# Kernel optimization log

Measured on AMD Instinct MI355X. Metric: run time of the kernel, lower is better.

The kernel has to match this reference:

```python
import jax, jax.numpy as jnp
import numpy as np
from jax import lax

ALPHA = 0.85
C1 = 0.01 ** 2
C2 = 0.03 ** 2


def _avg_pool3(x):
    # F.avg_pool2d(x, 3, 1, 1) with count_include_pad=True: zero-pad, divide by 9.
    s = lax.reduce_window(x, jnp.array(0.0, x.dtype), lax.add,
                          (1, 1, 3, 3), (1, 1, 1, 1),
                          [(0, 0), (0, 0), (1, 1), (1, 1)])
    return s / jnp.array(9.0, x.dtype)


def _ssim(x, y):
    mu_x = _avg_pool3(x)
    mu_y = _avg_pool3(y)
    sigma_x = jnp.clip(_avg_pool3(x * x) - mu_x * mu_x, 0.0, None)
    sigma_y = jnp.clip(_avg_pool3(y * y) - mu_y * mu_y, 0.0, None)
    sigma_xy = _avg_pool3(x * y) - mu_x * mu_y
    ssim_n = (2.0 * mu_x * mu_y + C1) * (2.0 * sigma_xy + C2)
    ssim_d = (mu_x * mu_x + mu_y * mu_y + C1) * (sigma_x + sigma_y + C2)
    return jnp.clip((1.0 - ssim_n / ssim_d) / 2.0, 0.0, 1.0)


def _warp_right(right_img, disp):
    # grid_sample(bilinear, border, align_corners=True) where y maps identically
    # to its own row -> a 1D horizontal bilinear gather at x_sample = x - disp.
    B, C, H, W = right_img.shape
    x_base = jnp.arange(W, dtype=disp.dtype).reshape(1, 1, 1, W)
    x_sample = x_base - disp                      # [B,1,H,W]
    xs = jnp.clip(x_sample, 0.0, W - 1.0)         # border padding
    x0 = jnp.floor(xs)
    w = xs - x0                                   # frac weight
    i0 = x0.astype(jnp.int32)
    i1 = jnp.minimum(i0 + 1, W - 1)
    i0b = jnp.broadcast_to(i0, (B, C, H, W))
    i1b = jnp.broadcast_to(i1, (B, C, H, W))
    g0 = jnp.take_along_axis(right_img, i0b, axis=3)
    g1 = jnp.take_along_axis(right_img, i1b, axis=3)
    warped = (1.0 - w) * g0 + w * g1              # w broadcasts over C
    valid = ((x_sample > 0) & (x_sample < W - 1)).astype(disp.dtype)
    return warped, valid


def setup_inputs() -> dict:
    key = jax.random.key(0)
    k1, k2, k3 = jax.random.split(key, 3)
    B, H, W = 8, 720, 1280
    disp = jax.random.normal(k1, (B, 1, H, W), dtype=jnp.float32)
    left_img = jax.random.uniform(k2, (B, 3, H, W), dtype=jnp.float32)
    right_img = jax.random.uniform(k3, (B, 3, H, W), dtype=jnp.float32)
    return {"disp": disp, "left_img": left_img, "right_img": right_img}


def reference(disp, left_img, right_img):
    right_warped, valid = _warp_right(right_img, disp)
    l1_err = jnp.mean(jnp.abs(left_img - right_warped), axis=1, keepdims=True)
    ssim_err = jnp.mean(_ssim(left_img, right_warped), axis=1, keepdims=True)
    photo_err = ALPHA * ssim_err + (1.0 - ALPHA) * l1_err
    n_valid = jnp.maximum(jnp.sum(valid), 1.0)
    return jnp.sum(photo_err * valid) / n_valid
```

## Files before the change

### kernel.cpp

```cpp
#include <hip/hip_runtime.h>


#define P_ALPHA 0.85f
#define P_C1 1e-4f
#define P_C2 9e-4f

constexpr int COLS  = 62;
constexpr int RPW   = 12;
constexpr int WAVES = 4;

__global__ __launch_bounds__(256)
void photo_loss_kernel(const float* __restrict__ disp,
                       const float* __restrict__ left,
                       const float* __restrict__ right,
                       float* __restrict__ acc,
                       int H, int W)
{
    __shared__ float redpv[WAVES];
    __shared__ float redv[WAVES];

    const int tid  = threadIdx.x;
    const int lane = tid & 63;
    const int w    = tid >> 6;
    const int b    = blockIdx.z;
    const int col  = blockIdx.x * COLS + lane - 1;
    const int rowStart = (blockIdx.y * WAVES + w) * RPW;

    const int planeHW = H * W;
    const float* __restrict__ dispb = disp  + b * planeHW;
    const float* __restrict__ L0 = left  + (b * 3 + 0) * planeHW;
    const float* __restrict__ L1 = left  + (b * 3 + 1) * planeHW;
    const float* __restrict__ L2 = left  + (b * 3 + 2) * planeHW;
    const float* __restrict__ R0 = right + (b * 3 + 0) * planeHW;
    const float* __restrict__ R1 = right + (b * 3 + 1) * planeHW;
    const float* __restrict__ R2 = right + (b * 3 + 2) * planeHW;

    const float wm1f = (float)(W - 1);
    const int   colC = min(max(col, 0), W - 1);
    const float colv = (col >= 0 && col < W) ? 1.f : 0.f;
    const float ocm  = (lane >= 1 && lane <= COLS && col < W) ? 1.f : 0.f;

    float rsx[3][3], rsy[3][3], rsxx[3][3], rsyy[3][3], rsxy[3][3];
    float l1r[3], vr[3];

    float sum_pv = 0.f, sum_v = 0.f;

    auto emit = [&](int cs) {
        const float inv9 = 1.f / 9.f;
        float ssim_sum = 0.f;
        #pragma unroll
        for (int c = 0; c < 3; ++c) {
            float mu_x = (rsx[c][0]  + rsx[c][1]  + rsx[c][2])  * inv9;
            float mu_y = (rsy[c][0]  + rsy[c][1]  + rsy[c][2])  * inv9;
            float exx  = (rsxx[c][0] + rsxx[c][1] + rsxx[c][2]) * inv9;
            float eyy  = (rsyy[c][0] + rsyy[c][1] + rsyy[c][2]) * inv9;
            float exy  = (rsxy[c][0] + rsxy[c][1] + rsxy[c][2]) * inv9;
            float sig_x  = fmaxf(exx - mu_x * mu_x, 0.f);
            float sig_y  = fmaxf(eyy - mu_y * mu_y, 0.f);
            float sig_xy = exy - mu_x * mu_y;
            float n  = (2.f * mu_x * mu_y + P_C1) * (2.f * sig_xy + P_C2);
            float dd = (mu_x * mu_x + mu_y * mu_y + P_C1) * (sig_x + sig_y + P_C2);
            float s  = (1.f - n * __builtin_amdgcn_rcpf(dd)) * 0.5f;
            s = fminf(fmaxf(s, 0.f), 1.f);
            ssim_sum += s;
        }
        float photo = P_ALPHA * (ssim_sum * (1.f / 3.f))
                    + (1.f - P_ALPHA) * (l1r[cs] * (1.f / 3.f));
        sum_pv += photo * vr[cs] * ocm;
        sum_v  += vr[cs] * ocm;
    };

    float dC, xC0, xC1, xC2;
    {
        const int r  = rowStart - 1;
        const int rc = min(max(r, 0), H - 1);
        const int off = rc * W + colC;
        dC = dispb[off]; xC0 = L0[off]; xC1 = L1[off]; xC2 = L2[off];
    }

    #pragma unroll
    for (int j = 0; j <= RPW + 2; ++j) {
        const int s = j % 3;
        const int r = rowStart - 1 + j;
        if (j <= RPW + 1) {
            const int   rc = min(max(r, 0), H - 1);
            const float rv = (r >= 0 && r < H) ? 1.f : 0.f;
            const float m  = rv * colv;

            const float xs  = (float)col - dC;
            const float xcl = fminf(fmaxf(xs, 0.f), wm1f);
            const float xf  = floorf(xcl);
            const float fr  = xcl - xf;
            const int   i0  = (int)xf;
            const int   i1  = min(i0 + 1, W - 1);
            const int   ro  = rc * W;
            const float g00 = R0[ro + i0], g01 = R0[ro + i1];
            const float g10 = R1[ro + i0], g11 = R1[ro + i1];
            const float g20 = R2[ro + i0], g21 = R2[ro + i1];

            float dN = 0.f, xN0 = 0.f, xN1 = 0.f, xN2 = 0.f;
            if (j <= RPW) {
                const int rn   = min(max(r + 1, 0), H - 1);
                const int offn = rn * W + colC;
                dN = dispb[offn]; xN0 = L0[offn]; xN1 = L1[offn]; xN2 = L2[offn];
            }

            if (j >= 3) emit((s + 1) % 3);

            const float omf = 1.f - fr;
            const float y0 = (omf * g00 + fr * g01) * m;
            const float y1 = (omf * g10 + fr * g11) * m;
            const float y2 = (omf * g20 + fr * g21) * m;
            const float x0 = xC0 * m;
            const float x1 = xC1 * m;
            const float x2 = xC2 * m;

            float xl, xr, yl, yr;
            xl = __shfl_up(x0, 1, 64); xr = __shfl_down(x0, 1, 64);
            yl = __shfl_up(y0, 1, 64); yr = __shfl_down(y0, 1, 64);
            rsx[0][s]  = xl + x0 + xr;
            rsy[0][s]  = yl + y0 + yr;
            rsxx[0][s] = xl * xl + x0 * x0 + xr * xr;
            rsyy[0][s] = yl * yl + y0 * y0 + yr * yr;
            rsxy[0][s] = xl * yl + x0 * y0 + xr * yr;

            xl = __shfl_up(x1, 1, 64); xr = __shfl_down(x1, 1, 64);
            yl = __shfl_up(y1, 1, 64); yr = __shfl_down(y1, 1, 64);
            rsx[1][s]  = xl + x1 + xr;
            rsy[1][s]  = yl + y1 + yr;
            rsxx[1][s] = xl * xl + x1 * x1 + xr * xr;
            rsyy[1][s] = yl * yl + y1 * y1 + yr * yr;
            rsxy[1][s] = xl * yl + x1 * y1 + xr * yr;

            xl = __shfl_up(x2, 1, 64); xr = __shfl_down(x2, 1, 64);
            yl = __shfl_up(y2, 1, 64); yr = __shfl_down(y2, 1, 64);
            rsx[2][s]  = xl + x2 + xr;
            rsy[2][s]  = yl + y2 + yr;
            rsxx[2][s] = xl * xl + x2 * x2 + xr * xr;
            rsyy[2][s] = yl * yl + y2 * y2 + yr * yr;
            rsxy[2][s] = xl * yl + x2 * y2 + xr * yr;

            l1r[s] = fabsf(x0 - y0) + fabsf(x1 - y1) + fabsf(x2 - y2);
            vr[s]  = (xs > 0.f && xs < wm1f) ? 1.f : 0.f;

            dC = dN; xC0 = xN0; xC1 = xN1; xC2 = xN2;
        } else {
            emit((s + 1) % 3);
        }
    }

    #pragma unroll
    for (int off = 32; off > 0; off >>= 1) {
        sum_pv += __shfl_down(sum_pv, off, 64);
        sum_v  += __shfl_down(sum_v,  off, 64);
    }
    if (lane == 0) { redpv[w] = sum_pv; redv[w] = sum_v; }
    __syncthreads();
    if (tid == 0) {
        atomicAdd(&acc[0], redpv[0] + redpv[1] + redpv[2] + redpv[3]);
        atomicAdd(&acc[1], redv[0]  + redv[1]  + redv[2]  + redv[3]);
    }
}

__global__ void photo_loss_finalize(const float* __restrict__ acc,
                                    float* __restrict__ out)
{
    out[0] = acc[0] / fmaxf(acc[1], 1.f);
}

extern "C" void kernel_launch(void* const* d_in, const int* in_sizes, int n_in,
                              void* d_out, int out_size, void* d_ws, size_t ws_size,
                              hipStream_t stream)
{
    const float* disp  = (const float*)d_in[0];
    const float* left  = (const float*)d_in[1];
    const float* right = (const float*)d_in[2];
    float* out = (float*)d_out;
    float* acc = (float*)d_ws;

    const int B = 8, H = 720, W = 1280;

    hipMemsetAsync(acc, 0, 2 * sizeof(float), stream);

    dim3 grid((W + COLS - 1) / COLS, H / (WAVES * RPW), B);
    dim3 block(256);
    photo_loss_kernel<<<grid, block, 0, stream>>>(disp, left, right, acc, H, W);
    photo_loss_finalize<<<1, 1, 0, stream>>>(acc, out);
}
```

Before: 242.2 us.

## Flatten grid to per-wave tasks, process two tasks per wave, constant-fold sizes

Replaces the 3D grid with a 1D grid in which each wave independently takes two strip tasks (column strip × 12-row band × batch), so the number of blocks and atomics is halved. Image dimensions become compile-time constants, and the kernel asks for 5 blocks per SM through launch bounds. The goal is lower per-block launch and reduction overhead plus cheaper address arithmetic. In exchange, the larger register pressure limit may cause spills, and the decomposition of waves into tasks changes locality between neighbouring strips.

New measurement: 256.8 us. +6.0%, slower.

```diff
diff --git a/kernel.cpp b/kernel.cpp
--- a/kernel.cpp
+++ b/kernel.cpp
@@ -5,147 +5,159 @@
 #define P_C1 1e-4f
 #define P_C2 9e-4f
 
-constexpr int COLS  = 62;
+constexpr int W_ = 1280, H_ = 720, HW_ = W_ * H_;
+constexpr int UCOLS = 62;
 constexpr int RPW   = 12;
-constexpr int WAVES = 4;
+constexpr int XS    = 21;
+constexpr int YS    = H_ / RPW;
+constexpr int TASKS = XS * YS * 8;
+constexpr int HALF  = TASKS / 2;
+constexpr int NB    = HALF / 4;
 
-__global__ __launch_bounds__(256)
+__global__ __launch_bounds__(256, 5)
 void photo_loss_kernel(const float* __restrict__ disp,
                        const float* __restrict__ left,
                        const float* __restrict__ right,
-                       float* __restrict__ acc,
-                       int H, int W)
+                       float* __restrict__ acc)
 {
-    __shared__ float redpv[WAVES];
-    __shared__ float redv[WAVES];
+    __shared__ float redpv[4], redv[4];
 
     const int tid  = threadIdx.x;
     const int lane = tid & 63;
-    const int w    = tid >> 6;
-    const int b    = blockIdx.z;
-    const int col  = blockIdx.x * COLS + lane - 1;
-    const int rowStart = (blockIdx.y * WAVES + w) * RPW;
-
-    const int planeHW = H * W;
-    const float* __restrict__ dispb = disp  + b * planeHW;
-    const float* __restrict__ L0 = left  + (b * 3 + 0) * planeHW;
-    const float* __restrict__ L1 = left  + (b * 3 + 1) * planeHW;
-    const float* __restrict__ L2 = left  + (b * 3 + 2) * planeHW;
-    const float* __restrict__ R0 = right + (b * 3 + 0) * planeHW;
-    const float* __restrict__ R1 = right + (b * 3 + 1) * planeHW;
-    const float* __restrict__ R2 = right + (b * 3 + 2) * planeHW;
-
-    const float wm1f = (float)(W - 1);
-    const int   colC = min(max(col, 0), W - 1);
-    const float colv = (col >= 0 && col < W) ? 1.f : 0.f;
-    const float ocm  = (lane >= 1 && lane <= COLS && col < W) ? 1.f : 0.f;
-
-    float rsx[3][3], rsy[3][3], rsxx[3][3], rsyy[3][3], rsxy[3][3];
-    float l1r[3], vr[3];
+    const int wv   = tid >> 6;
+    const int wgid = blockIdx.x * 4 + wv;
+    const float wm1 = (float)(W_ - 1);
 
     float sum_pv = 0.f, sum_v = 0.f;
 
-    auto emit = [&](int cs) {
-        const float inv9 = 1.f / 9.f;
-        float ssim_sum = 0.f;
+    for (int half = 0; half < 2; ++half) {
+        const int t   = wgid + half * HALF;
+        const int xs  = t % XS;
+        const int rem = t / XS;
+        const int ys  = rem % YS;
+        const int b   = rem / YS;
+
+        const int base = xs * UCOLS;
+        const int col  = base + lane - 1;
+        const int r0   = ys * RPW;
+
+        const float* __restrict__ dispb = disp + (size_t)b * HW_;
+        const float* __restrict__ L0 = left  + (size_t)(b * 3 + 0) * HW_;
+        const float* __restrict__ L1 = left  + (size_t)(b * 3 + 1) * HW_;
+        const float* __restrict__ L2 = left  + (size_t)(b * 3 + 2) * HW_;
+        const float* __restrict__ R0 = right + (size_t)(b * 3 + 0) * HW_;
+        const float* __restrict__ R1 = right + (size_t)(b * 3 + 1) * HW_;
+        const float* __restrict__ R2 = right + (size_t)(b * 3 + 2) * HW_;
+
+        const int   colC = min(max(col, 0), W_ - 1);
+        const float colv = (col >= 0 && col < W_) ? 1.f : 0.f;
+        const float ocm  = (lane >= 1 && lane <= UCOLS && col < W_) ? 1.f : 0.f;
+
+        float rsx[3][3], rsy[3][3], rsxx[3][3], rsyy[3][3], rsxy[3][3];
+        float l1r[3], vr[3];
+
+        auto emit = [&](int cs) {
+            const float inv9 = 1.f / 9.f;
+            float ssim_sum = 0.f;
+            #pragma unroll
+            for (int c = 0; c < 3; ++c) {
+                float mu_x = (rsx[c][0]  + rsx[c][1]  + rsx[c][2])  * inv9;
+                float mu_y = (rsy[c][0]  + rsy[c][1]  + rsy[c][2])  * inv9;
+                float exx  = (rsxx[c][0] + rsxx[c][1] + rsxx[c][2]) * inv9;
+                float eyy  = (rsyy[c][0] + rsyy[c][1] + rsyy[c][2]) * inv9;
+                float exy  = (rsxy[c][0] + rsxy[c][1] + rsxy[c][2]) * inv9;
+                float sig_x  = fmaxf(exx - mu_x * mu_x, 0.f);
+                float sig_y  = fmaxf(eyy - mu_y * mu_y, 0.f);
+                float sig_xy = exy - mu_x * mu_y;
+                float n  = (2.f * mu_x * mu_y + P_C1) * (2.f * sig_xy + P_C2);
+                float dd = (mu_x * mu_x + mu_y * mu_y + P_C1) * (sig_x + sig_y + P_C2);
+                float s  = (1.f - n * __builtin_amdgcn_rcpf(dd)) * 0.5f;
+                s = fminf(fmaxf(s, 0.f), 1.f);
+                ssim_sum += s;
+            }
+            float photo = P_ALPHA * (ssim_sum * (1.f / 3.f))
+                        + (1.f - P_ALPHA) * (l1r[cs] * (1.f / 3.f));
+            sum_pv += photo * vr[cs] * ocm;
+            sum_v  += vr[cs] * ocm;
+        };
+
+        float dC, xC0, xC1, xC2;
+        {
+            const int rc  = max(r0 - 1, 0);
+            const int off = rc * W_ + colC;
+            dC = dispb[off]; xC0 = L0[off]; xC1 = L1[off]; xC2 = L2[off];
+        }
+
         #pragma unroll
-        for (int c = 0; c < 3; ++c) {
-            float mu_x = (rsx[c][0]  + rsx[c][1]  + rsx[c][2])  * inv9;
-            float mu_y = (rsy[c][0]  + rsy[c][1]  + rsy[c][2])  * inv9;
-            float exx  = (rsxx[c][0] + rsxx[c][1] + rsxx[c][2]) * inv9;
-            float eyy  = (rsyy[c][0] + rsyy[c][1] + rsyy[c][2]) * inv9;
-            float exy  = (rsxy[c][0] + rsxy[c][1] + rsxy[c][2]) * inv9;
-            float sig_x  = fmaxf(exx - mu_x * mu_x, 0.f);
-            float sig_y  = fmaxf(eyy - mu_y * mu_y, 0.f);
-            float sig_xy = exy - mu_x * mu_y;
-            float n  = (2.f * mu_x * mu_y + P_C1) * (2.f * sig_xy + P_C2);
-            float dd = (mu_x * mu_x + mu_y * mu_y + P_C1) * (sig_x + sig_y + P_C2);
-            float s  = (1.f - n * __builtin_amdgcn_rcpf(dd)) * 0.5f;
-            s = fminf(fmaxf(s, 0.f), 1.f);
-            ssim_sum += s;
-        }
-        float photo = P_ALPHA * (ssim_sum * (1.f / 3.f))
-                    + (1.f - P_ALPHA) * (l1r[cs] * (1.f / 3.f));
-        sum_pv += photo * vr[cs] * ocm;
-        sum_v  += vr[cs] * ocm;
-    };
+        for (int j = 0; j <= RPW + 2; ++j) {
+            const int s = j % 3;
+            const int r = r0 - 1 + j;
+            if (j <= RPW + 1) {
+                const int   rc = min(max(r, 0), H_ - 1);
+                const float rv = (r >= 0 && r < H_) ? 1.f : 0.f;
+                const float m  = rv * colv;
 
-    float dC, xC0, xC1, xC2;
-    {
-        const int r  = rowStart - 1;
-        const int rc = min(max(r, 0), H - 1);
-        const int off = rc * W + colC;
-        dC = dispb[off]; xC0 = L0[off]; xC1 = L1[off]; xC2 = L2[off];
-    }
+                const float xsm = (float)col - dC;
+                const float xcl = fminf(fmaxf(xsm, 0.f), wm1);
+                const float xf  = floorf(xcl);
+                const float fr  = xcl - xf;
+                const int   i0  = (int)xf;
+                const int   i1  = min(i0 + 1, W_ - 1);
+                const int   ro  = rc * W_;
+                const float g00 = R0[ro + i0], g01 = R0[ro + i1];
+                const float g10 = R1[ro + i0], g11 = R1[ro + i1];
+                const float g20 = R2[ro + i0], g21 = R2[ro + i1];
 
-    #pragma unroll
-    for (int j = 0; j <= RPW + 2; ++j) {
-        const int s = j % 3;
-        const int r = rowStart - 1 + j;
-        if (j <= RPW + 1) {
-            const int   rc = min(max(r, 0), H - 1);
-            const float rv = (r >= 0 && r < H) ? 1.f : 0.f;
-            const float m  = rv * colv;
+                float dN = 0.f, xN0 = 0.f, xN1 = 0.f, xN2 = 0.f;
+                if (j <= RPW) {
+                    const int rn   = min(max(r + 1, 0), H_ - 1);
+                    const int offn = rn * W_ + colC;
+                    dN = dispb[offn];
+                    xN0 = L0[offn]; xN1 = L1[offn]; xN2 = L2[offn];
+                }
 
-            const float xs  = (float)col - dC;
-            const float xcl = fminf(fmaxf(xs, 0.f), wm1f);
-            const float xf  = floorf(xcl);
-            const float fr  = xcl - xf;
-            const int   i0  = (int)xf;
-            const int   i1  = min(i0 + 1, W - 1);
-            const int   ro  = rc * W;
-            const float g00 = R0[ro + i0], g01 = R0[ro + i1];
-            const float g10 = R1[ro + i0], g11 = R1[ro + i1];
-            const float g20 = R2[ro + i0], g21 = R2[ro + i1];
+                if (j >= 3) emit((s + 1) % 3);
 
-            float dN = 0.f, xN0 = 0.f, xN1 = 0.f, xN2 = 0.f;
-            if (j <= RPW) {
-                const int rn   = min(max(r + 1, 0), H - 1);
-                const int offn = rn * W + colC;
-                dN = dispb[offn]; xN0 = L0[offn]; xN1 = L1[offn]; xN2 = L2[offn];
+                const float omf = 1.f - fr;
+                const float y0 = (omf * g00 + fr * g01) * m;
+                const float y1 = (omf * g10 + fr * g11) * m;
+                const float y2 = (omf * g20 + fr * g21) * m;
+                const float x0 = xC0 * m;
+                const float x1 = xC1 * m;
+                const float x2 = xC2 * m;
+
+                float xl, xr, yl, yr;
+                xl = __shfl_up(x0, 1, 64); xr = __shfl_down(x0, 1, 64);
+                yl = __shfl_up(y0, 1, 64); yr = __shfl_down(y0, 1, 64);
+                rsx[0][s]  = xl + x0 + xr;
+                rsy[0][s]  = yl + y0 + yr;
+                rsxx[0][s] = xl * xl + x0 * x0 + xr * xr;
+                rsyy[0][s] = yl * yl + y0 * y0 + yr * yr;
+                rsxy[0][s] = xl * yl + x0 * y0 + xr * yr;
+
+                xl = __shfl_up(x1, 1, 64); xr = __shfl_down(x1, 1, 64);
+                yl = __shfl_up(y1, 1, 64); yr = __shfl_down(y1, 1, 64);
+                rsx[1][s]  = xl + x1 + xr;
+                rsy[1][s]  = yl + y1 + yr;
+                rsxx[1][s] = xl * xl + x1 * x1 + xr * xr;
+                rsyy[1][s] = yl * yl + y1 * y1 + yr * yr;
+                rsxy[1][s] = xl * yl + x1 * y1 + xr * yr;
+
+                xl = __shfl_up(x2, 1, 64); xr = __shfl_down(x2, 1, 64);
+                yl = __shfl_up(y2, 1, 64); yr = __shfl_down(y2, 1, 64);
+                rsx[2][s]  = xl + x2 + xr;
+                rsy[2][s]  = yl + y2 + yr;
+                rsxx[2][s] = xl * xl + x2 * x2 + xr * xr;
+                rsyy[2][s] = yl * yl + y2 * y2 + yr * yr;
+                rsxy[2][s] = xl * yl + x2 * y2 + xr * yr;
+
+                l1r[s] = fabsf(x0 - y0) + fabsf(x1 - y1) + fabsf(x2 - y2);
+                vr[s]  = (xsm > 0.f && xsm < wm1) ? 1.f : 0.f;
+
+                dC = dN; xC0 = xN0; xC1 = xN1; xC2 = xN2;
+            } else {
+                emit((s + 1) % 3);
             }
-
-            if (j >= 3) emit((s + 1) % 3);
-
-            const float omf = 1.f - fr;
-            const float y0 = (omf * g00 + fr * g01) * m;
-            const float y1 = (omf * g10 + fr * g11) * m;
-            const float y2 = (omf * g20 + fr * g21) * m;
-            const float x0 = xC0 * m;
-            const float x1 = xC1 * m;
-            const float x2 = xC2 * m;
-
-            float xl, xr, yl, yr;
-            xl = __shfl_up(x0, 1, 64); xr = __shfl_down(x0, 1, 64);
-            yl = __shfl_up(y0, 1, 64); yr = __shfl_down(y0, 1, 64);
-            rsx[0][s]  = xl + x0 + xr;
-            rsy[0][s]  = yl + y0 + yr;
-            rsxx[0][s] = xl * xl + x0 * x0 + xr * xr;
-            rsyy[0][s] = yl * yl + y0 * y0 + yr * yr;
-            rsxy[0][s] = xl * yl + x0 * y0 + xr * yr;
-
-            xl = __shfl_up(x1, 1, 64); xr = __shfl_down(x1, 1, 64);
-            yl = __shfl_up(y1, 1, 64); yr = __shfl_down(y1, 1, 64);
-            rsx[1][s]  = xl + x1 + xr;
-            rsy[1][s]  = yl + y1 + yr;
-            rsxx[1][s] = xl * xl + x1 * x1 + xr * xr;
-            rsyy[1][s] = yl * yl + y1 * y1 + yr * yr;
-            rsxy[1][s] = xl * yl + x1 * y1 + xr * yr;
-
-            xl = __shfl_up(x2, 1, 64); xr = __shfl_down(x2, 1, 64);
-            yl = __shfl_up(y2, 1, 64); yr = __shfl_down(y2, 1, 64);
-            rsx[2][s]  = xl + x2 + xr;
-            rsy[2][s]  = yl + y2 + yr;
-            rsxx[2][s] = xl * xl + x2 * x2 + xr * xr;
-            rsyy[2][s] = yl * yl + y2 * y2 + yr * yr;
-            rsxy[2][s] = xl * yl + x2 * y2 + xr * yr;
-
-            l1r[s] = fabsf(x0 - y0) + fabsf(x1 - y1) + fabsf(x2 - y2);
-            vr[s]  = (xs > 0.f && xs < wm1f) ? 1.f : 0.f;
-
-            dC = dN; xC0 = xN0; xC1 = xN1; xC2 = xN2;
-        } else {
-            emit((s + 1) % 3);
         }
     }
 
@@ -154,7 +166,7 @@
         sum_pv += __shfl_down(sum_pv, off, 64);
         sum_v  += __shfl_down(sum_v,  off, 64);
     }
-    if (lane == 0) { redpv[w] = sum_pv; redv[w] = sum_v; }
+    if (lane == 0) { redpv[wv] = sum_pv; redv[wv] = sum_v; }
     __syncthreads();
     if (tid == 0) {
         atomicAdd(&acc[0], redpv[0] + redpv[1] + redpv[2] + redpv[3]);
@@ -178,12 +190,10 @@
     float* out = (float*)d_out;
     float* acc = (float*)d_ws;
 
-    const int B = 8, H = 720, W = 1280;
-
     hipMemsetAsync(acc, 0, 2 * sizeof(float), stream);
 
-    dim3 grid((W + COLS - 1) / COLS, H / (WAVES * RPW), B);
+    dim3 grid(NB);
     dim3 block(256);
-    photo_loss_kernel<<<grid, block, 0, stream>>>(disp, left, right, acc, H, W);
+    photo_loss_kernel<<<grid, block, 0, stream>>>(disp, left, right, acc);
     photo_loss_finalize<<<1, 1, 0, stream>>>(acc, out);
 }
```
